# Kernel tuning notes

Measured on AMD Instinct MI355X. Metric: run time of the kernel, lower is better.

## Reference

```python
import jax, jax.numpy as jnp
import numpy as np
import math

# Model config (see init_kwargs)
E = 1024   # emb_size
H = 8      # ffwd_num_head
D = 128    # ffwd_head_size (E == H*D)
NE = 16    # ffwd_num_expert
A = 2      # ffwd_num_expert_active
S = 256    # ffwd_expert_size
B = 2      # batch_size_fwd
T = 2048   # context_window
NUM_BLOCK = 12


def setup_inputs() -> dict:
    key = jax.random.key(0)
    ks = jax.random.split(key, 5)
    x = jax.random.normal(ks[0], (B, T, E), jnp.float32)
    # fc_in_fused: Linear(E, 4E+NE, bias=False), torch weight shape (out,in)
    w_in = 0.02 * jax.random.normal(ks[1], (4 * E + NE, E), jnp.float32)
    # fc_out_fused: Linear(2E, E), std 0.02/sqrt(num_block)
    w_out = (0.02 / math.sqrt(NUM_BLOCK)) * jax.random.normal(ks[2], (E, 2 * E), jnp.float32)
    # k_ffwd/v_ffwd: original (1,H,NE*S,D); stored here as (NE,H,S,D) for per-expert scan
    k_ffwd = 0.02 * jax.random.normal(ks[3], (NE, H, S, D), jnp.float32)
    v_ffwd = 0.02 * jax.random.normal(ks[4], (NE, H, S, D), jnp.float32)
    return {"x": x, "w_in": w_in, "w_out": w_out, "k_ffwd": k_ffwd, "v_ffwd": v_ffwd}


def _rope(t):
    # Standard half-split RoPE, base 10000. t: (B,T,H,D)
    half = t.shape[-1] // 2
    inv_freq = 1.0 / (10000.0 ** (jnp.arange(half, dtype=jnp.float32) / half))
    ang = jnp.arange(t.shape[1], dtype=jnp.float32)[:, None] * inv_freq  # (T, half)
    cos = jnp.cos(ang)[None, :, None, :]
    sin = jnp.sin(ang)[None, :, None, :]
    t1, t2 = t[..., :half], t[..., half:]
    return jnp.concatenate([t1 * cos - t2 * sin, t1 * sin + t2 * cos], axis=-1)


def reference(x, w_in, w_out, k_ffwd, v_ffwd):
    Bx, Tx, _ = x.shape
    h = x @ w_in.T  # (B,T,4E+NE)
    q_f, q_a, k_a, v_a, router_logits = jnp.split(h, [E, 2 * E, 3 * E, 4 * E], axis=-1)

    # top-k routing (order of the k slots is irrelevant: outputs are summed)
    gate_logits, assign = jax.lax.top_k(router_logits, A)  # (B,T,A)
    gate = jax.nn.sigmoid(gate_logits)

    # --- attention half: causal softmax attention, scale 1/sqrt(D), with RoPE ---
    q = _rope(q_a.reshape(Bx, Tx, H, D))
    k = _rope(k_a.reshape(Bx, Tx, H, D))
    v = v_a.reshape(Bx, Tx, H, D)
    scores = jnp.einsum('bqhd,bkhd->bhqk', q, k) / math.sqrt(D)
    causal = jnp.tril(jnp.ones((Tx, Tx), dtype=bool))
    scores = jnp.where(causal, scores, -jnp.inf)
    p = jax.nn.softmax(scores, axis=-1)
    attn_out = jnp.einsum('bhqk,bkhd->bqhd', p, v).reshape(Bx, Tx, E)

    # --- MoE-FFN half, expressed as attention with score_mod log1p(gelu):
    # exp(lse)*softmax recovers sum_s (1+gelu(q.k_s)) v_s; subtracting sum_s v_s
    # leaves sum_s gelu(q.k_s) v_s over the assigned expert's slots. ---
    qf = q_f.reshape(Bx, Tx, H, D)

    def step(acc, ekv):
        e, ke, ve = ekv  # ke, ve: (H,S,D)
        s = jnp.einsum('bthd,hsd->bths', qf, ke)
        a = jax.nn.gelu(s, approximate=False)  # torch F.gelu default = exact erf
        o = jnp.einsum('bths,hsd->bthd', a, ve)
        g = jnp.sum(jnp.where(assign == e, gate, 0.0), axis=-1)  # (B,T)
        return acc + g[..., None, None] * o, None

    acc0 = jnp.zeros((Bx, Tx, H, D), x.dtype)
    ffwd_out, _ = jax.lax.scan(step, acc0, (jnp.arange(NE), k_ffwd, v_ffwd))
    ffwd_out = ffwd_out.reshape(Bx, Tx, E)

    out = jnp.concatenate([attn_out, ffwd_out], axis=-1) @ w_out.T  # (B,T,E)
    return out
```

## Files before the change

kernel.cpp:

```cpp
#include <hip/hip_runtime.h>
#include <hip/hip_bf16.h>
#include <math.h>

#define E 1024
#define NEXP 16
#define HH 8
#define DD 128
#define SS 256
#define BB 2
#define TT 2048
#define BT 4096

typedef __attribute__((ext_vector_type(8))) short bf16x8;
typedef __attribute__((ext_vector_type(4))) float f32x4;

#define GLDS16(g, s) __builtin_amdgcn_global_load_lds( \
    (const __attribute__((address_space(1))) void*)(g), \
    (__attribute__((address_space(3))) void*)(s), 16, 0, 0)

__device__ __forceinline__ ushort f2b(float f) {
    union { float f; unsigned u; } v; v.f = f;
    unsigned r = (v.u + 0x7FFFu + ((v.u >> 16) & 1u)) >> 16;
    return (ushort)r;
}
__device__ __forceinline__ float b2f(ushort u) {
    union { unsigned u; float f; } v; v.u = ((unsigned)u) << 16;
    return v.f;
}
__device__ __forceinline__ float gelu_fast(float x) {
    float u2 = x * x;
    float tu = x * (1.5957691216f + 0.0713548163f * u2);
    float e = __expf(tu);
    float sig = 1.f - __builtin_amdgcn_rcpf(e + 1.f);
    return x * sig;
}

__global__ void cvtk_swz(const float* __restrict__ in, ushort* __restrict__ outp,
                         int kshift, int n)
{
    int i = (blockIdx.x * blockDim.x + threadIdx.x) * 8;
    if (i >= n) return;
    int row = i >> kshift;
    int colb = (i - (row << kshift)) * 2;
    float4 f0 = *(const float4*)(in + i);
    float4 f1 = *(const float4*)(in + i + 4);
    ushort4 u0, u1;
    u0.x = f2b(f0.x); u0.y = f2b(f0.y); u0.z = f2b(f0.z); u0.w = f2b(f0.w);
    u1.x = f2b(f1.x); u1.y = f2b(f1.y); u1.z = f2b(f1.z); u1.w = f2b(f1.w);
    char* dst = (char*)outp + ((size_t)row << (kshift + 1)) + (colb ^ ((row & 7) << 4));
    *(ushort4*)dst = u0;
    *(ushort4*)(dst + 8) = u1;
}

template<int BF16OUT>
__global__ __launch_bounds__(256) void gemm_bf16(
    const ushort* __restrict__ A, int lda,
    const ushort* __restrict__ B, int ldb,
    void* __restrict__ Cv, int ldc, int K)
{
    __shared__ ushort As[128 * 64];
    __shared__ ushort Bs[128 * 64];
    const int t = threadIdx.x;
    const int l = t & 63, w = t >> 6;
    const int m0 = blockIdx.y * 128, n0 = blockIdx.x * 128;
    const int wr = w >> 1, wc = w & 1;
    const int fr = l & 15, fg = l >> 4;

    const int srow = w * 32 + (l >> 3);
    const int sboff = (l & 7) * 16;
    const char* Ag = (const char*)A + ((size_t)(m0 + srow) * lda) * 2 + sboff;
    const char* Bg = (const char*)B + ((size_t)(n0 + srow) * ldb) * 2 + sboff;
    const int aswz = (fr & 7) << 4;

    f32x4 acc[4][4];
    #pragma unroll
    for (int i = 0; i < 4; ++i)
        #pragma unroll
        for (int j = 0; j < 4; ++j) { acc[i][j][0]=0.f; acc[i][j][1]=0.f; acc[i][j][2]=0.f; acc[i][j][3]=0.f; }

    for (int k0b = 0; k0b < K * 2; k0b += 128) {
        #pragma unroll
        for (int i = 0; i < 4; ++i) {
            GLDS16(Ag + (size_t)(i * 8) * lda * 2 + k0b, (char*)As + (w * 32 + i * 8) * 128);
            GLDS16(Bg + (size_t)(i * 8) * ldb * 2 + k0b, (char*)Bs + (w * 32 + i * 8) * 128);
        }
        __syncthreads();
        #pragma unroll
        for (int ksub = 0; ksub < 2; ++ksub) {
            bf16x8 a[4], b[4];
            #pragma unroll
            for (int mi = 0; mi < 4; ++mi)
                a[mi] = *(const bf16x8*)((const char*)As + (wr * 64 + mi * 16 + fr) * 128 + ((ksub * 64 + fg * 16) ^ aswz));
            #pragma unroll
            for (int ni = 0; ni < 4; ++ni)
                b[ni] = *(const bf16x8*)((const char*)Bs + (wc * 64 + ni * 16 + fr) * 128 + ((ksub * 64 + fg * 16) ^ aswz));
            #pragma unroll
            for (int mi = 0; mi < 4; ++mi)
                #pragma unroll
                for (int ni = 0; ni < 4; ++ni)
                    acc[mi][ni] = __builtin_amdgcn_mfma_f32_16x16x32_bf16(a[mi], b[ni], acc[mi][ni], 0, 0, 0);
        }
        __syncthreads();
    }
    #pragma unroll
    for (int mi = 0; mi < 4; ++mi)
        #pragma unroll
        for (int ni = 0; ni < 4; ++ni) {
            const int row = m0 + wr * 64 + mi * 16 + fg * 4;
            const int col = n0 + wc * 64 + ni * 16 + fr;
            #pragma unroll
            for (int r = 0; r < 4; ++r) {
                if (BF16OUT)
                    ((ushort*)Cv)[(size_t)(row + r) * ldc + col] = f2b(acc[mi][ni][r]);
                else
                    ((float*)Cv)[(size_t)(row + r) * ldc + col] = acc[mi][ni][r];
            }
        }
}

__global__ __launch_bounds__(256) void gemm1_fused(
    const ushort* __restrict__ A, const ushort* __restrict__ B,
    ushort* __restrict__ hbq,
    ushort* __restrict__ qb, ushort* __restrict__ kb,
    ushort* __restrict__ vtb)
{
    __shared__ ushort sh[128 * 128];
    ushort* As = sh;
    ushort* Bs = sh + 128 * 64;
    const int t = threadIdx.x;
    const int l = t & 63, w = t >> 6;
    const int m0 = blockIdx.y * 128, n0 = blockIdx.x * 128;
    const int wr = w >> 1, wc = w & 1;
    const int fr = l & 15, fg = l >> 4;

    const int srow = w * 32 + (l >> 3);
    const int sboff = (l & 7) * 16;
    const char* Ag = (const char*)A + ((size_t)(m0 + srow) * 1024) * 2 + sboff;
    const char* Bg = (const char*)B + ((size_t)(n0 + srow) * 1024) * 2 + sboff;
    const int aswz = (fr & 7) << 4;

    f32x4 acc[4][4];
    #pragma unroll
    for (int i = 0; i < 4; ++i)
        #pragma unroll
        for (int j = 0; j < 4; ++j) { acc[i][j][0]=0.f; acc[i][j][1]=0.f; acc[i][j][2]=0.f; acc[i][j][3]=0.f; }

    for (int k0b = 0; k0b < 2048; k0b += 128) {
        #pragma unroll
        for (int i = 0; i < 4; ++i) {
            GLDS16(Ag + (size_t)(i * 8) * 2048 + k0b, (char*)As + (w * 32 + i * 8) * 128);
            GLDS16(Bg + (size_t)(i * 8) * 2048 + k0b, (char*)Bs + (w * 32 + i * 8) * 128);
        }
        __syncthreads();
        #pragma unroll
        for (int ksub = 0; ksub < 2; ++ksub) {
            bf16x8 a[4], b[4];
            #pragma unroll
            for (int mi = 0; mi < 4; ++mi)
                a[mi] = *(const bf16x8*)((const char*)As + (wr * 64 + mi * 16 + fr) * 128 + ((ksub * 64 + fg * 16) ^ aswz));
            #pragma unroll
            for (int ni = 0; ni < 4; ++ni)
                b[ni] = *(const bf16x8*)((const char*)Bs + (wc * 64 + ni * 16 + fr) * 128 + ((ksub * 64 + fg * 16) ^ aswz));
            #pragma unroll
            for (int mi = 0; mi < 4; ++mi)
                #pragma unroll
                for (int ni = 0; ni < 4; ++ni)
                    acc[mi][ni] = __builtin_amdgcn_mfma_f32_16x16x32_bf16(a[mi], b[ni], acc[mi][ni], 0, 0, 0);
        }
        __syncthreads();
    }

    const int region = blockIdx.x >> 3;
    const int hd = blockIdx.x & 7;

    if (region == 0) {
        #pragma unroll
        for (int mi = 0; mi < 4; ++mi)
            #pragma unroll
            for (int ni = 0; ni < 4; ++ni) {
                const int row = m0 + wr * 64 + mi * 16 + fg * 4;
                const int col = n0 + wc * 64 + ni * 16 + fr;
                #pragma unroll
                for (int r = 0; r < 4; ++r)
                    hbq[(size_t)(row + r) * 1024 + col] = f2b(acc[mi][ni][r]);
            }
    } else if (region == 3) {
        #pragma unroll
        for (int mi = 0; mi < 4; ++mi) {
            const int rowg = m0 + wr * 64 + mi * 16 + fg * 4;
            const int tok = rowg & 2047, bt = rowg >> 11;
            const int bh = bt * 8 + hd;
            #pragma unroll
            for (int ni = 0; ni < 4; ++ni) {
                const int d = wc * 64 + ni * 16 + fr;
                ushort4 u;
                u.x = f2b(acc[mi][ni][0]); u.y = f2b(acc[mi][ni][1]);
                u.z = f2b(acc[mi][ni][2]); u.w = f2b(acc[mi][ni][3]);
                char* dst = (char*)vtb + (size_t)(bh * 128 + d) * 4096
                          + (tok >> 6) * 128 + ((2 * (tok & 63)) ^ ((d & 7) << 4));
                *(ushort4*)dst = u;
            }
        }
    } else {
        #pragma unroll
        for (int mi = 0; mi < 4; ++mi)
            #pragma unroll
            for (int ni = 0; ni < 4; ++ni) {
                const int rl = wr * 64 + mi * 16 + fg * 4;
                const int cl = wc * 64 + ni * 16 + fr;
                #pragma unroll
                for (int r = 0; r < 4; ++r)
                    sh[(rl + r) * 128 + cl] = f2b(acc[mi][ni][r]);
            }
        __syncthreads();
        ushort* outb = (region == 1) ? qb : kb;
        #pragma unroll
        for (int it = 0; it < 4; ++it) {
            const int item = it * 256 + t;
            const int rloc = item >> 3, g = item & 7;
            const int rowg = m0 + rloc;
            const int tok = rowg & 2047, bt = rowg >> 11;
            const int sw = (tok & 7) << 4;
            char* rowbase = (char*)outb + ((size_t)((bt * 8 + hd) * 2048 + tok)) * 256;
            ushort lo[8], hi[8];
            #pragma unroll
            for (int jj = 0; jj < 8; ++jj) {
                const int j = g * 8 + jj;
                float t1 = b2f(sh[rloc * 128 + j]);
                float t2 = b2f(sh[rloc * 128 + 64 + j]);
                float invf = __expf(-(float)j * (9.210340371976184f / 64.f));
                float ang = (float)tok * invf;
                float s, c;
                sincosf(ang, &s, &c);
                lo[jj] = f2b(t1 * c - t2 * s);
                hi[jj] = f2b(t1 * s + t2 * c);
            }
            *(ushort4*)(rowbase + ((16 * g) ^ sw))        = *(ushort4*)&lo[0];
            *(ushort4*)(rowbase + (((16 * g) ^ sw) + 8))  = *(ushort4*)&lo[4];
            *(ushort4*)(rowbase + ((16 * g + 128) ^ sw))       = *(ushort4*)&hi[0];
            *(ushort4*)(rowbase + (((16 * g + 128) ^ sw) + 8)) = *(ushort4*)&hi[4];
        }
    }
}

__global__ __launch_bounds__(256) void router_logits(
    const float* __restrict__ x, const float* __restrict__ w_in,
    float* __restrict__ gval, int* __restrict__ eidx, ushort* __restrict__ xb)
{
    const int m = blockIdx.x * 4 + (threadIdx.x >> 6);
    const int lane = threadIdx.x & 63;

    const float* xp = x + (size_t)m * 1024 + lane * 4;
    float4 xv0 = *(const float4*)(xp);
    float4 xv1 = *(const float4*)(xp + 256);
    float4 xv2 = *(const float4*)(xp + 512);
    float4 xv3 = *(const float4*)(xp + 768);

    {
        const int swrow = (m & 7) << 4;
        char* xrow = (char*)xb + (size_t)m * 2048;
        ushort4 u;
        u.x = f2b(xv0.x); u.y = f2b(xv0.y); u.z = f2b(xv0.z); u.w = f2b(xv0.w);
        *(ushort4*)(xrow + ((lane * 8 + 0 * 512) ^ swrow)) = u;
        u.x = f2b(xv1.x); u.y = f2b(xv1.y); u.z = f2b(xv1.z); u.w = f2b(xv1.w);
        *(ushort4*)(xrow + ((lane * 8 + 1 * 512) ^ swrow)) = u;
        u.x = f2b(xv2.x); u.y = f2b(xv2.y); u.z = f2b(xv2.z); u.w = f2b(xv2.w);
        *(ushort4*)(xrow + ((lane * 8 + 2 * 512) ^ swrow)) = u;
        u.x = f2b(xv3.x); u.y = f2b(xv3.y); u.z = f2b(xv3.z); u.w = f2b(xv3.w);
        *(ushort4*)(xrow + ((lane * 8 + 3 * 512) ^ swrow)) = u;
    }

    float p[16];
    #pragma unroll
    for (int e = 0; e < 16; ++e) {
        const float* wp = w_in + (size_t)(4096 + e) * 1024 + lane * 4;
        float4 w0 = *(const float4*)(wp);
        float4 w1 = *(const float4*)(wp + 256);
        float4 w2 = *(const float4*)(wp + 512);
        float4 w3 = *(const float4*)(wp + 768);
        float s0 = xv0.x * w0.x + xv0.y * w0.y + xv0.z * w0.z + xv0.w * w0.w;
        float s1 = xv1.x * w1.x + xv1.y * w1.y + xv1.z * w1.z + xv1.w * w1.w;
        float s2 = xv2.x * w2.x + xv2.y * w2.y + xv2.z * w2.z + xv2.w * w2.w;
        float s3 = xv3.x * w3.x + xv3.y * w3.y + xv3.z * w3.z + xv3.w * w3.w;
        p[e] = (s0 + s1) + (s2 + s3);
    }
    #pragma unroll
    for (int d = 1; d < 64; d <<= 1) {
        #pragma unroll
        for (int e = 0; e < 16; ++e)
            p[e] += __shfl_xor(p[e], d);
    }
    float best = -1e30f; int bi = 0;
    #pragma unroll
    for (int e = 0; e < 16; ++e)
        if (p[e] > best) { best = p[e]; bi = e; }
    float best2 = -1e30f; int bi2 = 0;
    #pragma unroll
    for (int e = 0; e < 16; ++e)
        if (e != bi && p[e] > best2) { best2 = p[e]; bi2 = e; }

    if (lane == 0) {
        gval[m * 2 + 0] = 1.f / (1.f + __expf(-best));
        gval[m * 2 + 1] = 1.f / (1.f + __expf(-best2));
        eidx[m * 2 + 0] = bi;
        eidx[m * 2 + 1] = bi2;
    }
}

__global__ __launch_bounds__(256) void build_lists(
    const int* __restrict__ eidx,
    int* __restrict__ counts, int* __restrict__ plist)
{
    const int e = blockIdx.x;
    const int t = threadIdx.x;
    const int w = t >> 6, lane = t & 63;
    __shared__ int wbase[4];
    __shared__ int running;
    if (t == 0) running = 0;
    __syncthreads();
    for (int c = 0; c < 2 * BT; c += 256) {
        const int p = c + t;
        const bool match = (eidx[p] == e);
        unsigned long long mask = __ballot(match);
        int lpre = __popcll(mask & ((lane == 63) ? 0x7FFFFFFFFFFFFFFFull
                                                 : ((1ull << lane) - 1ull)));
        if (lane == 0) wbase[w] = __popcll(mask);
        __syncthreads();
        int pre = running;
        #pragma unroll
        for (int i = 0; i < 4; ++i) if (i < w) pre += wbase[i];
        const int tot = wbase[0] + wbase[1] + wbase[2] + wbase[3];
        if (match) plist[e * BT + pre + lpre] = p;
        __syncthreads();
        if (t == 0) running += tot;
        __syncthreads();
    }
    if (t == 0) counts[e] = running;
}

__global__ __launch_bounds__(256) void cvt_kv(
    const float* __restrict__ kf, const float* __restrict__ vf,
    ushort* __restrict__ kfb, ushort* __restrict__ vtf)
{
    __shared__ float T[64][132];
    int eh = blockIdx.y, st = blockIdx.x;
    int s0 = st * 64;
    int t = threadIdx.x;
    const float* kbp = kf + (size_t)eh * SS * DD + (size_t)s0 * DD;
    const float* vbp = vf + (size_t)eh * SS * DD + (size_t)s0 * DD;
    for (int i = t; i < 64 * 32; i += 256) {
        int r = i >> 5, c4 = i & 31;
        float4 f = *(const float4*)(kbp + (size_t)r * DD + c4 * 4);
        ushort4 u;
        u.x = f2b(f.x); u.y = f2b(f.y); u.z = f2b(f.z); u.w = f2b(f.w);
        *(ushort4*)((char*)kfb + ((size_t)eh * 256 + s0 + r) * 256 + ((c4 * 8) ^ ((r & 7) << 4))) = u;
    }
    for (int i = t; i < 64 * 32; i += 256) {
        int r = i >> 5, c4 = i & 31;
        float4 f = *(const float4*)(vbp + (size_t)r * DD + c4 * 4);
        T[r][c4 * 4 + 0] = f.x; T[r][c4 * 4 + 1] = f.y;
        T[r][c4 * 4 + 2] = f.z; T[r][c4 * 4 + 3] = f.w;
    }
    __syncthreads();
    int g = t >> 4, fr = t & 15;
    #pragma unroll
    for (int dd = 0; dd < 8; ++dd) {
        int d = g + dd * 16;
        ushort4 u;
        u.x = f2b(T[4 * fr + 0][d]); u.y = f2b(T[4 * fr + 1][d]);
        u.z = f2b(T[4 * fr + 2][d]); u.w = f2b(T[4 * fr + 3][d]);
        size_t ob = ((size_t)eh * 128 + d) * 512 + s0 * 2;
        *(ushort4*)((char*)vtf + ob + ((8 * fr) ^ ((d & 7) << 4))) = u;
    }
}

__global__ __launch_bounds__(512, 1) void attn_mfma(
    const ushort* __restrict__ qb, const ushort* __restrict__ kb,
    const ushort* __restrict__ vtb, ushort* __restrict__ catb)
{
    __shared__ ushort Ks[2][128 * 128];
    __shared__ ushort Vs[2][128 * 128];
    __shared__ ushort Ps[8][16 * 72];
    __shared__ float  LlS[8][16];

    const int t = threadIdx.x, l = t & 63, w = t >> 6;
    const int fr = l & 15, fg = l >> 4;
    const int wl = w & 3, hh = w >> 2;
    const int lin = blockIdx.x;
    const int bh = (lin & 7) * 2 + (lin >> 7);
    const int tpair = (lin >> 3) & 15;
    const int swz = (fr & 7) << 4;
    ushort* Pw = (ushort*)Ps[w];

    #pragma unroll 1
    for (int pass = 0; pass < 2; ++pass) {
        const int qt = pass ? (31 - tpair) : tpair;
        const int qbase = qt * 64;
        const int nkt = (qt + 2) >> 1;
        const int qg = qbase + wl * 16 + fg * 4;

        bf16x8 qreg[4];
        {
            const char* qrow = (const char*)qb + ((size_t)(bh * 2048 + qbase + wl * 16 + fr)) * 256;
            #pragma unroll
            for (int ks = 0; ks < 4; ++ks)
                qreg[ks] = *(const bf16x8*)(qrow + ((ks * 64 + fg * 16) ^ swz));
        }
        {
            const char* ksrc = (const char*)kb + ((size_t)(bh * 2048 + w * 16)) * 256;
            const char* vsrc = (const char*)vtb + ((size_t)(bh * 128 + w * 16)) * 4096;
            #pragma unroll
            for (int i = 0; i < 4; ++i) {
                GLDS16(ksrc + (size_t)(i * 4 + (l >> 4)) * 256 + (l & 15) * 16,
                       (char*)Ks[0] + (w * 16 + i * 4) * 256);
                GLDS16(vsrc + (size_t)(i * 4 + (l >> 4)) * 4096 + (l & 15) * 16,
                       (char*)Vs[0] + (w * 16 + i * 4) * 256);
            }
        }

        f32x4 po[8];
        #pragma unroll
        for (int i = 0; i < 8; ++i) { po[i][0]=0.f; po[i][1]=0.f; po[i][2]=0.f; po[i][3]=0.f; }
        float lrow[4] = {0.f, 0.f, 0.f, 0.f};

        asm volatile("s_waitcnt vmcnt(0)" ::: "memory");
        __syncthreads();

        for (int kt = 0; kt < nkt; ++kt) {
            const int cur = kt & 1;
            if (kt + 1 < nkt) {
                const int kvn = (kt + 1) * 128;
                const char* ksrc = (const char*)kb + ((size_t)(bh * 2048 + kvn + w * 16)) * 256;
                const char* vsrc = (const char*)vtb + ((size_t)(bh * 128 + w * 16)) * 4096 + kvn * 2;
                #pragma unroll
                for (int i = 0; i < 4; ++i) {
                    GLDS16(ksrc + (size_t)(i * 4 + (l >> 4)) * 256 + (l & 15) * 16,
                           (char*)Ks[cur ^ 1] + (w * 16 + i * 4) * 256);
                    GLDS16(vsrc + (size_t)(i * 4 + (l >> 4)) * 4096 + (l & 15) * 16,
                           (char*)Vs[cur ^ 1] + (w * 16 + i * 4) * 256);
                }
            }
            const int kvb = kt * 128;

            f32x4 s[4];
            #pragma unroll
            for (int i = 0; i < 4; ++i) { s[i][0]=0.f; s[i][1]=0.f; s[i][2]=0.f; s[i][3]=0.f; }
            __builtin_amdgcn_s_setprio(1);
            #pragma unroll
            for (int ks = 0; ks < 4; ++ks) {
                #pragma unroll
                for (int fn = 0; fn < 4; ++fn) {
                    const int brow = hh * 64 + fn * 16 + fr;
                    bf16x8 bb = *(const bf16x8*)((const char*)Ks[cur] + brow * 256 + ((ks * 64 + fg * 16) ^ swz));
                    s[fn] = __builtin_amdgcn_mfma_f32_16x16x32_bf16(qreg[ks], bb, s[fn], 0, 0, 0);
                }
            }
            __builtin_amdgcn_s_setprio(0);

            const int colbase = kvb + hh * 64;
            const bool needmask = (colbase + 64 > qbase + wl * 16);
            float ps[4] = {0.f, 0.f, 0.f, 0.f};
            #pragma unroll
            for (int fn = 0; fn < 4; ++fn)
                #pragma unroll
                for (int r = 0; r < 4; ++r) {
                    float v = s[fn][r] * 0.08838834764831845f;
                    bool masked = needmask && (colbase + fn * 16 + fr > qg + r);
                    float p = masked ? 0.f : __expf(v);
                    ps[r] += p;
                    Pw[(fg * 4 + r) * 72 + fn * 16 + fr] = f2b(p);
                }
            #pragma unroll
            for (int r = 0; r < 4; ++r) {
                float s2 = ps[r];
                s2 += __shfl_xor(s2, 1);
                s2 += __shfl_xor(s2, 2);
                s2 += __shfl_xor(s2, 4);
                s2 += __shfl_xor(s2, 8);
                lrow[r] += s2;
            }

            asm volatile("s_waitcnt lgkmcnt(0)" ::: "memory");
            __builtin_amdgcn_sched_barrier(0);

            __builtin_amdgcn_s_setprio(1);
            #pragma unroll
            for (int ks2 = 0; ks2 < 2; ++ks2) {
                bf16x8 pa = *(const bf16x8*)((const char*)Pw + fr * 144 + ks2 * 64 + fg * 16);
                #pragma unroll
                for (int fn2 = 0; fn2 < 8; ++fn2) {
                    const int vrow = fn2 * 16 + fr;
                    bf16x8 bv = *(const bf16x8*)((const char*)Vs[cur] + vrow * 256 + ((hh * 128 + ks2 * 64 + fg * 16) ^ swz));
                    po[fn2] = __builtin_amdgcn_mfma_f32_16x16x32_bf16(pa, bv, po[fn2], 0, 0, 0);
                }
            }
            __builtin_amdgcn_s_setprio(0);

            asm volatile("s_waitcnt vmcnt(0)" ::: "memory");
            __syncthreads();
        }

        if (fr == 0) {
            #pragma unroll
            for (int r = 0; r < 4; ++r)
                LlS[w][fg * 4 + r] = lrow[r];
        }
        __syncthreads();
        float linv[4];
        #pragma unroll
        for (int r = 0; r < 4; ++r)
            linv[r] = 1.f / (lrow[r] + LlS[w ^ 4][fg * 4 + r]);
        float* PO = (float*)&Ks[0][0];
        if (hh == 1) {
            #pragma unroll
            for (int fn2 = 0; fn2 < 8; ++fn2)
                #pragma unroll
                for (int r = 0; r < 4; ++r)
                    PO[(wl * 16 + fg * 4 + r) * 128 + fn2 * 16 + fr] = po[fn2][r];
        }
        __syncthreads();
        if (hh == 0) {
            const int mg = (bh >> 3) * 2048 + qbase + wl * 16 + fg * 4;
            #pragma unroll
            for (int r = 0; r < 4; ++r) {
                const int rswz = ((mg + r) & 7) << 4;
                #pragma unroll
                for (int fn2 = 0; fn2 < 8; ++fn2) {
                    float v = po[fn2][r] + PO[(wl * 16 + fg * 4 + r) * 128 + fn2 * 16 + fr];
                    int colb = ((bh & 7) * 128 + fn2 * 16 + fr) * 2;
                    *(ushort*)((char*)catb + (size_t)(mg + r) * 4096 + (colb ^ rswz)) = f2b(v * linv[r]);
                }
            }
        }
        __syncthreads();
    }
}

__global__ __launch_bounds__(256, 1) void ffn_mfma2(
    const ushort* __restrict__ hbq,
    const float* __restrict__ gv,
    const int* __restrict__ counts,
    const int* __restrict__ plist,
    const ushort* __restrict__ kfb, const ushort* __restrict__ vtf,
    ushort* __restrict__ pairout)
{
    __shared__ ushort Ks[256 * 128];
    __shared__ ushort Vs[128 * 256];
    __shared__ ushort Qs[64 * 128];
    __shared__ ushort Ps[4][16 * 72];

    const int t = threadIdx.x, l = t & 63, w = t >> 6;
    const int fr = l & 15, fg = l >> 4;
    const int half = blockIdx.x, hd = blockIdx.y, e = blockIdx.z;
    const int eh = e * HH + hd;
    const int n_e = counts[e];

    {
        const char* kbase = (const char*)kfb + (size_t)eh * 65536;
        const char* vbase = (const char*)vtf + (size_t)eh * 65536;
        #pragma unroll
        for (int i = 0; i < 16; ++i) {
            GLDS16(kbase + (w * 64 + i * 4) * 256 + l * 16, (char*)Ks + (w * 64 + i * 4) * 256);
            GLDS16(vbase + w * 16384 + i * 1024 + l * 16, (char*)Vs + w * 16384 + i * 1024);
        }
    }
    __syncthreads();

    const int arow = w * 16 + fr;
    const int aswz = (arow & 7) << 4;
    ushort* Pw = (ushort*)Ps[w];
    const int rl4 = l >> 4;
    const int lb = (l & 15) * 16;

    for (int tb = half * 64; tb < n_e; tb += 128) {
        #pragma unroll
        for (int i = 0; i < 4; ++i) {
            int row = w * 16 + i * 4 + rl4;
            int gr = tb + row;
            int p = plist[e * BT + min(gr, n_e - 1)];
            int m = p >> 1;
            const char* src = (const char*)hbq + (size_t)m * 2048 + hd * 256 + (lb ^ ((row & 7) << 4));
            GLDS16(src, (char*)Qs + (w * 16 + i * 4) * 256);
        }
        asm volatile("s_waitcnt vmcnt(0)" ::: "memory");

        f32x4 po[8];
        #pragma unroll
        for (int i = 0; i < 8; ++i) { po[i][0]=0.f; po[i][1]=0.f; po[i][2]=0.f; po[i][3]=0.f; }

        #pragma unroll
        for (int kt = 0; kt < 4; ++kt) {
            const int kvb = kt * 64;
            f32x4 sA[4];
            #pragma unroll
            for (int i = 0; i < 4; ++i) { sA[i][0]=0.f; sA[i][1]=0.f; sA[i][2]=0.f; sA[i][3]=0.f; }
            #pragma unroll
            for (int ks = 0; ks < 4; ++ks) {
                bf16x8 aa = *(const bf16x8*)((const char*)Qs + arow * 256 + ((ks * 64 + fg * 16) ^ aswz));
                #pragma unroll
                for (int fn = 0; fn < 4; ++fn) {
                    const int brow = kvb + fn * 16 + fr;
                    bf16x8 bb = *(const bf16x8*)((const char*)Ks + brow * 256 + ((ks * 64 + fg * 16) ^ ((brow & 7) << 4)));
                    sA[fn] = __builtin_amdgcn_mfma_f32_16x16x32_bf16(aa, bb, sA[fn], 0, 0, 0);
                }
            }
            #pragma unroll
            for (int fn = 0; fn < 4; ++fn)
                #pragma unroll
                for (int r = 0; r < 4; ++r)
                    Pw[(fg * 4 + r) * 72 + fn * 16 + fr] = f2b(gelu_fast(sA[fn][r]));
            asm volatile("s_waitcnt lgkmcnt(0)" ::: "memory");
            #pragma unroll
            for (int ks2 = 0; ks2 < 2; ++ks2) {
                bf16x8 pa = *(const bf16x8*)((const char*)Pw + fr * 144 + ks2 * 64 + fg * 16);
                #pragma unroll
                for (int fn2 = 0; fn2 < 8; ++fn2) {
                    const int vrow = fn2 * 16 + fr;
                    bf16x8 bv = *(const bf16x8*)((const char*)Vs + vrow * 512 + kt * 128 + ((ks2 * 64 + fg * 16) ^ ((vrow & 7) << 4)));
                    po[fn2] = __builtin_amdgcn_mfma_f32_16x16x32_bf16(pa, bv, po[fn2], 0, 0, 0);
                }
            }
        }
        const int rloc = w * 16 + fg * 4;
        #pragma unroll
        for (int r = 0; r < 4; ++r) {
            int gr = tb + rloc + r;
            if (gr < n_e) {
                int p = plist[e * BT + gr];
                float g = gv[p];
                #pragma unroll
                for (int fn2 = 0; fn2 < 8; ++fn2)
                    pairout[(size_t)p * 1024 + hd * DD + fn2 * 16 + fr] = f2b(g * po[fn2][r]);
            }
        }
    }
}

__global__ void combine_kernel(const ushort* __restrict__ po, ushort* __restrict__ catb)
{
    int i = blockIdx.x * blockDim.x + threadIdx.x;
    if (i >= BT * 128) return;
    int m = i >> 7, c = i & 127;
    const ushort* a = po + (size_t)(2 * m) * 1024 + c * 8;
    const ushort* b = po + (size_t)(2 * m + 1) * 1024 + c * 8;
    ushort4 a0 = *(const ushort4*)a, a1 = *(const ushort4*)(a + 4);
    ushort4 b0 = *(const ushort4*)b, b1 = *(const ushort4*)(b + 4);
    ushort4 o0, o1;
    o0.x = f2b(b2f(a0.x) + b2f(b0.x)); o0.y = f2b(b2f(a0.y) + b2f(b0.y));
    o0.z = f2b(b2f(a0.z) + b2f(b0.z)); o0.w = f2b(b2f(a0.w) + b2f(b0.w));
    o1.x = f2b(b2f(a1.x) + b2f(b1.x)); o1.y = f2b(b2f(a1.y) + b2f(b1.y));
    o1.z = f2b(b2f(a1.z) + b2f(b1.z)); o1.w = f2b(b2f(a1.w) + b2f(b1.w));
    char* dst = (char*)catb + (size_t)m * 4096 + 2048 + ((c * 16) ^ ((m & 7) << 4));
    *(ushort4*)dst = o0;
    *(ushort4*)(dst + 8) = o1;
}

extern "C" void kernel_launch(void* const* d_in, const int* in_sizes, int n_in,
                              void* d_out, int out_size, void* d_ws, size_t ws_size,
                              hipStream_t stream)
{
    const float* x     = (const float*)d_in[0];
    const float* w_in  = (const float*)d_in[1];
    const float* w_out = (const float*)d_in[2];
    const float* kf    = (const float*)d_in[3];
    const float* vf    = (const float*)d_in[4];
    float* out = (float*)d_out;

    char* W = (char*)d_ws;
    ushort* hbq     = (ushort*)(W + 0);
    ushort* xb      = (ushort*)(W + 33554432);
    ushort* wib     = (ushort*)(W + 41943040);
    ushort* kfb     = xb;
    ushort* vtf     = wib;
    ushort* wob     = (ushort*)(W + 50331648);
    ushort* qb2     = (ushort*)(W + 54525952);
    ushort* kb2     = (ushort*)(W + 62914560);
    ushort* vtb     = (ushort*)(W + 71303168);
    ushort* catb    = (ushort*)(W + 79691776);
    ushort* pairout = (ushort*)(W + 96468992);
    float*  gv      = (float*)(W + 113246208);
    int*    counts  = (int*)(W + 113278976);
    int*    plist   = (int*)(W + 113279040);
    int*    eidx    = (int*)(W + 113541184);

    cvtk_swz<<<2048, 256, 0, stream>>>(w_in, wib, 10, 4096 * 1024);
    cvtk_swz<<<1024, 256, 0, stream>>>(w_out, wob, 11, 1024 * 2048);

    router_logits<<<BT / 4, 256, 0, stream>>>(x, w_in, gv, eidx, xb);
    build_lists<<<NEXP, 256, 0, stream>>>(eidx, counts, plist);

    gemm1_fused<<<dim3(32, 32), 256, 0, stream>>>(xb, wib, hbq, qb2, kb2, vtb);

    cvt_kv<<<dim3(4, NEXP * HH), 256, 0, stream>>>(kf, vf, kfb, vtf);

    attn_mfma<<<dim3(256), 512, 0, stream>>>(qb2, kb2, vtb, catb);

    ffn_mfma2<<<dim3(2, HH, NEXP), 256, 0, stream>>>(hbq, gv, counts, plist, kfb, vtf, pairout);
    combine_kernel<<<2048, 256, 0, stream>>>(pairout, catb);

    gemm_bf16<0><<<dim3(8, 32), 256, 0, stream>>>(catb, 2048, wob, 2048, out, 1024, 2048);
}
```

Baseline: 234.1 us.

## Widen gemm1 tile to 128x256 and apply RoPE directly from registers

The fused input GEMM now uses a 128x256 output tile, so each wave covers a full 128-wide head and A-tile loads are reused across twice as many columns, halving the grid. Because each wave holds both halves of a head, the RoPE epilogue rotates straight from accumulator registers and drops the LDS staging round-trip and its extra barrier. In exchange it doubles the accumulator registers, which may reduce occupancy, and writes q/k with scattered 2-byte stores instead of vectorized 8-byte stores. Only 512 blocks remain, which may underfill the GPU.

Result: slower. 809.0 us (+245.6%).

```diff
diff --git a/kernel.cpp b/kernel.cpp
--- a/kernel.cpp
+++ b/kernel.cpp
@@ -124,62 +124,63 @@
     ushort* __restrict__ qb, ushort* __restrict__ kb,
     ushort* __restrict__ vtb)
 {
-    __shared__ ushort sh[128 * 128];
-    ushort* As = sh;
-    ushort* Bs = sh + 128 * 64;
+    __shared__ ushort As[128 * 64];
+    __shared__ ushort Bs[256 * 64];
     const int t = threadIdx.x;
     const int l = t & 63, w = t >> 6;
-    const int m0 = blockIdx.y * 128, n0 = blockIdx.x * 128;
+    const int m0 = blockIdx.y * 128, n0 = blockIdx.x * 256;
     const int wr = w >> 1, wc = w & 1;
     const int fr = l & 15, fg = l >> 4;
 
-    const int srow = w * 32 + (l >> 3);
+    const int lrow = l >> 3;
     const int sboff = (l & 7) * 16;
-    const char* Ag = (const char*)A + ((size_t)(m0 + srow) * 1024) * 2 + sboff;
-    const char* Bg = (const char*)B + ((size_t)(n0 + srow) * 1024) * 2 + sboff;
+    const char* Ag = (const char*)A + ((size_t)(m0 + w * 32 + lrow) * 1024) * 2 + sboff;
+    const char* Bg = (const char*)B + ((size_t)(n0 + w * 64 + lrow) * 1024) * 2 + sboff;
     const int aswz = (fr & 7) << 4;
 
-    f32x4 acc[4][4];
+    f32x4 acc[4][8];
     #pragma unroll
     for (int i = 0; i < 4; ++i)
         #pragma unroll
-        for (int j = 0; j < 4; ++j) { acc[i][j][0]=0.f; acc[i][j][1]=0.f; acc[i][j][2]=0.f; acc[i][j][3]=0.f; }
+        for (int j = 0; j < 8; ++j) { acc[i][j][0]=0.f; acc[i][j][1]=0.f; acc[i][j][2]=0.f; acc[i][j][3]=0.f; }
 
     for (int k0b = 0; k0b < 2048; k0b += 128) {
         #pragma unroll
-        for (int i = 0; i < 4; ++i) {
+        for (int i = 0; i < 4; ++i)
             GLDS16(Ag + (size_t)(i * 8) * 2048 + k0b, (char*)As + (w * 32 + i * 8) * 128);
-            GLDS16(Bg + (size_t)(i * 8) * 2048 + k0b, (char*)Bs + (w * 32 + i * 8) * 128);
-        }
+        #pragma unroll
+        for (int i = 0; i < 8; ++i)
+            GLDS16(Bg + (size_t)(i * 8) * 2048 + k0b, (char*)Bs + (w * 64 + i * 8) * 128);
         __syncthreads();
         #pragma unroll
         for (int ksub = 0; ksub < 2; ++ksub) {
-            bf16x8 a[4], b[4];
+            bf16x8 a[4], b[8];
             #pragma unroll
             for (int mi = 0; mi < 4; ++mi)
                 a[mi] = *(const bf16x8*)((const char*)As + (wr * 64 + mi * 16 + fr) * 128 + ((ksub * 64 + fg * 16) ^ aswz));
             #pragma unroll
-            for (int ni = 0; ni < 4; ++ni)
-                b[ni] = *(const bf16x8*)((const char*)Bs + (wc * 64 + ni * 16 + fr) * 128 + ((ksub * 64 + fg * 16) ^ aswz));
+            for (int ni = 0; ni < 8; ++ni)
+                b[ni] = *(const bf16x8*)((const char*)Bs + (wc * 128 + ni * 16 + fr) * 128 + ((ksub * 64 + fg * 16) ^ aswz));
             #pragma unroll
             for (int mi = 0; mi < 4; ++mi)
                 #pragma unroll
-                for (int ni = 0; ni < 4; ++ni)
+                for (int ni = 0; ni < 8; ++ni)
                     acc[mi][ni] = __builtin_amdgcn_mfma_f32_16x16x32_bf16(a[mi], b[ni], acc[mi][ni], 0, 0, 0);
         }
         __syncthreads();
     }
 
-    const int region = blockIdx.x >> 3;
-    const int hd = blockIdx.x & 7;
+    const int region = blockIdx.x >> 2;
+    const int creg = blockIdx.x & 3;
+    const int hd = creg * 2 + wc;
 
     if (region == 0) {
         #pragma unroll
         for (int mi = 0; mi < 4; ++mi)
             #pragma unroll
-            for (int ni = 0; ni < 4; ++ni) {
+            for (int ni = 0; ni < 8; ++ni) {
                 const int row = m0 + wr * 64 + mi * 16 + fg * 4;
-                const int col = n0 + wc * 64 + ni * 16 + fr;
+                const int col = n0 + wc * 128 + ni * 16 + fr;
                 #pragma unroll
                 for (int r = 0; r < 4; ++r)
                     hbq[(size_t)(row + r) * 1024 + col] = f2b(acc[mi][ni][r]);
@@ -191,8 +192,8 @@
             const int tok = rowg & 2047, bt = rowg >> 11;
             const int bh = bt * 8 + hd;
             #pragma unroll
-            for (int ni = 0; ni < 4; ++ni) {
-                const int d = wc * 64 + ni * 16 + fr;
+            for (int ni = 0; ni < 8; ++ni) {
+                const int d = ni * 16 + fr;
                 ushort4 u;
                 u.x = f2b(acc[mi][ni][0]); u.y = f2b(acc[mi][ni][1]);
                 u.z = f2b(acc[mi][ni][2]); u.w = f2b(acc[mi][ni][3]);
@@ -202,43 +203,32 @@
             }
         }
     } else {
-        #pragma unroll
-        for (int mi = 0; mi < 4; ++mi)
-            #pragma unroll
-            for (int ni = 0; ni < 4; ++ni) {
-                const int rl = wr * 64 + mi * 16 + fg * 4;
-                const int cl = wc * 64 + ni * 16 + fr;
-                #pragma unroll
-                for (int r = 0; r < 4; ++r)
-                    sh[(rl + r) * 128 + cl] = f2b(acc[mi][ni][r]);
-            }
-        __syncthreads();
         ushort* outb = (region == 1) ? qb : kb;
-        #pragma unroll
-        for (int it = 0; it < 4; ++it) {
-            const int item = it * 256 + t;
-            const int rloc = item >> 3, g = item & 7;
-            const int rowg = m0 + rloc;
-            const int tok = rowg & 2047, bt = rowg >> 11;
-            const int sw = (tok & 7) << 4;
-            char* rowbase = (char*)outb + ((size_t)((bt * 8 + hd) * 2048 + tok)) * 256;
-            ushort lo[8], hi[8];
-            #pragma unroll
-            for (int jj = 0; jj < 8; ++jj) {
-                const int j = g * 8 + jj;
-                float t1 = b2f(sh[rloc * 128 + j]);
-                float t2 = b2f(sh[rloc * 128 + 64 + j]);
-                float invf = __expf(-(float)j * (9.210340371976184f / 64.f));
-                float ang = (float)tok * invf;
-                float s, c;
-                sincosf(ang, &s, &c);
-                lo[jj] = f2b(t1 * c - t2 * s);
-                hi[jj] = f2b(t1 * s + t2 * c);
-            }
-            *(ushort4*)(rowbase + ((16 * g) ^ sw))        = *(ushort4*)&lo[0];
-            *(ushort4*)(rowbase + (((16 * g) ^ sw) + 8))  = *(ushort4*)&lo[4];
-            *(ushort4*)(rowbase + ((16 * g + 128) ^ sw))       = *(ushort4*)&hi[0];
-            *(ushort4*)(rowbase + (((16 * g + 128) ^ sw) + 8)) = *(ushort4*)&hi[4];
+        float invfs[4];
+        #pragma unroll
+        for (int ni = 0; ni < 4; ++ni)
+            invfs[ni] = __expf(-(float)(ni * 16 + fr) * (9.210340371976184f / 64.f));
+        #pragma unroll
+        for (int mi = 0; mi < 4; ++mi) {
+            const int rowg0 = m0 + wr * 64 + mi * 16 + fg * 4;
+            #pragma unroll
+            for (int r = 0; r < 4; ++r) {
+                const int rowg = rowg0 + r;
+                const int tok = rowg & 2047, bt = rowg >> 11;
+                const int sw = (tok & 7) << 4;
+                char* rowbase = (char*)outb + ((size_t)((bt * 8 + hd) * 2048 + tok)) * 256;
+                #pragma unroll
+                for (int ni = 0; ni < 4; ++ni) {
+                    const int j = ni * 16 + fr;
+                    float t1 = acc[mi][ni][r];
+                    float t2 = acc[mi][ni + 4][r];
+                    float ang = (float)tok * invfs[ni];
+                    float s, c;
+                    sincosf(ang, &s, &c);
+                    *(ushort*)(rowbase + ((2 * j) ^ sw))         = f2b(t1 * c - t2 * s);
+                    *(ushort*)(rowbase + ((2 * j + 128) ^ sw))   = f2b(t1 * s + t2 * c);
+                }
+            }
         }
     }
 }
@@ -689,7 +679,7 @@
     router_logits<<<BT / 4, 256, 0, stream>>>(x, w_in, gv, eidx, xb);
     build_lists<<<NEXP, 256, 0, stream>>>(eidx, counts, plist);
 
-    gemm1_fused<<<dim3(32, 32), 256, 0, stream>>>(xb, wib, hbq, qb2, kb2, vtb);
+    gemm1_fused<<<dim3(16, 32), 256, 0, stream>>>(xb, wib, hbq, qb2, kb2, vtb);
 
     cvt_kv<<<dim3(4, NEXP * HH), 256, 0, stream>>>(kf, vf, kfb, vtf);
 
```

## Merge weight/KV conversion kernels and fuse expert-pair combine into output GEMM

Applied to the files above, without the earlier changes.

Three conversion launches (w_in, w_out, k/v) are merged into one prep kernel; kfb/vtf get dedicated workspace so k/v conversion no longer waits on gemm1. The combine kernel is removed, and the final GEMM now sums the two expert-pair rows of pairout while loading the second half of its K dimension into shared memory. This removes two launches and a round trip through catb's FFN half. The cost is that the FFN half of the GEMM uses synchronous register loads instead of async global-to-LDS loads, which may stall the MFMA loop.

New measurement: 238.0 us. Within noise of the previous version (+1.7%).

```diff
diff --git a/kernel.cpp b/kernel.cpp
--- a/kernel.cpp
+++ b/kernel.cpp
@@ -35,87 +35,64 @@
     return x * sig;
 }
 
-__global__ void cvtk_swz(const float* __restrict__ in, ushort* __restrict__ outp,
-                         int kshift, int n)
+__global__ __launch_bounds__(256) void prep(
+    const float* __restrict__ w_in, const float* __restrict__ w_out,
+    const float* __restrict__ kf, const float* __restrict__ vf,
+    ushort* __restrict__ wib, ushort* __restrict__ wob,
+    ushort* __restrict__ kfb, ushort* __restrict__ vtf)
 {
-    int i = (blockIdx.x * blockDim.x + threadIdx.x) * 8;
-    if (i >= n) return;
-    int row = i >> kshift;
-    int colb = (i - (row << kshift)) * 2;
-    float4 f0 = *(const float4*)(in + i);
-    float4 f1 = *(const float4*)(in + i + 4);
-    ushort4 u0, u1;
-    u0.x = f2b(f0.x); u0.y = f2b(f0.y); u0.z = f2b(f0.z); u0.w = f2b(f0.w);
-    u1.x = f2b(f1.x); u1.y = f2b(f1.y); u1.z = f2b(f1.z); u1.w = f2b(f1.w);
-    char* dst = (char*)outp + ((size_t)row << (kshift + 1)) + (colb ^ ((row & 7) << 4));
-    *(ushort4*)dst = u0;
-    *(ushort4*)(dst + 8) = u1;
-}
-
-template<int BF16OUT>
-__global__ __launch_bounds__(256) void gemm_bf16(
-    const ushort* __restrict__ A, int lda,
-    const ushort* __restrict__ B, int ldb,
-    void* __restrict__ Cv, int ldc, int K)
-{
-    __shared__ ushort As[128 * 64];
-    __shared__ ushort Bs[128 * 64];
+    __shared__ float T[64][132];
+    const int bx = blockIdx.x;
     const int t = threadIdx.x;
-    const int l = t & 63, w = t >> 6;
-    const int m0 = blockIdx.y * 128, n0 = blockIdx.x * 128;
-    const int wr = w >> 1, wc = w & 1;
-    const int fr = l & 15, fg = l >> 4;
-
-    const int srow = w * 32 + (l >> 3);
-    const int sboff = (l & 7) * 16;
-    const char* Ag = (const char*)A + ((size_t)(m0 + srow) * lda) * 2 + sboff;
-    const char* Bg = (const char*)B + ((size_t)(n0 + srow) * ldb) * 2 + sboff;
-    const int aswz = (fr & 7) << 4;
-
-    f32x4 acc[4][4];
+
+    if (bx < 3072) {
+        const float* in;
+        ushort* outp;
+        int kshift, i;
+        if (bx < 2048) { in = w_in;  outp = wib; kshift = 10; i = (bx * 256 + t) * 8; }
+        else           { in = w_out; outp = wob; kshift = 11; i = ((bx - 2048) * 256 + t) * 8; }
+        int row = i >> kshift;
+        int colb = (i - (row << kshift)) * 2;
+        float4 f0 = *(const float4*)(in + i);
+        float4 f1 = *(const float4*)(in + i + 4);
+        ushort4 u0, u1;
+        u0.x = f2b(f0.x); u0.y = f2b(f0.y); u0.z = f2b(f0.z); u0.w = f2b(f0.w);
+        u1.x = f2b(f1.x); u1.y = f2b(f1.y); u1.z = f2b(f1.z); u1.w = f2b(f1.w);
+        char* dst = (char*)outp + ((size_t)row << (kshift + 1)) + (colb ^ ((row & 7) << 4));
+        *(ushort4*)dst = u0;
+        *(ushort4*)(dst + 8) = u1;
+        return;
+    }
+
+    const int idx = bx - 3072;
+    const int st = idx & 3, eh = idx >> 2;
+    const int s0 = st * 64;
+    const float* kbp = kf + (size_t)eh * SS * DD + (size_t)s0 * DD;
+    const float* vbp = vf + (size_t)eh * SS * DD + (size_t)s0 * DD;
+    for (int i = t; i < 64 * 32; i += 256) {
+        int r = i >> 5, c4 = i & 31;
+        float4 f = *(const float4*)(kbp + (size_t)r * DD + c4 * 4);
+        ushort4 u;
+        u.x = f2b(f.x); u.y = f2b(f.y); u.z = f2b(f.z); u.w = f2b(f.w);
+        *(ushort4*)((char*)kfb + ((size_t)eh * 256 + s0 + r) * 256 + ((c4 * 8) ^ ((r & 7) << 4))) = u;
+    }
+    for (int i = t; i < 64 * 32; i += 256) {
+        int r = i >> 5, c4 = i & 31;
+        float4 f = *(const float4*)(vbp + (size_t)r * DD + c4 * 4);
+        T[r][c4 * 4 + 0] = f.x; T[r][c4 * 4 + 1] = f.y;
+        T[r][c4 * 4 + 2] = f.z; T[r][c4 * 4 + 3] = f.w;
+    }
+    __syncthreads();
+    int g = t >> 4, fr = t & 15;
     #pragma unroll
-    for (int i = 0; i < 4; ++i)
-        #pragma unroll
-        for (int j = 0; j < 4; ++j) { acc[i][j][0]=0.f; acc[i][j][1]=0.f; acc[i][j][2]=0.f; acc[i][j][3]=0.f; }
-
-    for (int k0b = 0; k0b < K * 2; k0b += 128) {
-        #pragma unroll
-        for (int i = 0; i < 4; ++i) {
-            GLDS16(Ag + (size_t)(i * 8) * lda * 2 + k0b, (char*)As + (w * 32 + i * 8) * 128);
-            GLDS16(Bg + (size_t)(i * 8) * ldb * 2 + k0b, (char*)Bs + (w * 32 + i * 8) * 128);
-        }
-        __syncthreads();
-        #pragma unroll
-        for (int ksub = 0; ksub < 2; ++ksub) {
-            bf16x8 a[4], b[4];
-            #pragma unroll
-            for (int mi = 0; mi < 4; ++mi)
-                a[mi] = *(const bf16x8*)((const char*)As + (wr * 64 + mi * 16 + fr) * 128 + ((ksub * 64 + fg * 16) ^ aswz));
-            #pragma unroll
-            for (int ni = 0; ni < 4; ++ni)
-                b[ni] = *(const bf16x8*)((const char*)Bs + (wc * 64 + ni * 16 + fr) * 128 + ((ksub * 64 + fg * 16) ^ aswz));
-            #pragma unroll
-            for (int mi = 0; mi < 4; ++mi)
-                #pragma unroll
-                for (int ni = 0; ni < 4; ++ni)
-                    acc[mi][ni] = __builtin_amdgcn_mfma_f32_16x16x32_bf16(a[mi], b[ni], acc[mi][ni], 0, 0, 0);
-        }
-        __syncthreads();
-    }
-    #pragma unroll
-    for (int mi = 0; mi < 4; ++mi)
-        #pragma unroll
-        for (int ni = 0; ni < 4; ++ni) {
-            const int row = m0 + wr * 64 + mi * 16 + fg * 4;
-            const int col = n0 + wc * 64 + ni * 16 + fr;
-            #pragma unroll
-            for (int r = 0; r < 4; ++r) {
-                if (BF16OUT)
-                    ((ushort*)Cv)[(size_t)(row + r) * ldc + col] = f2b(acc[mi][ni][r]);
-                else
-                    ((float*)Cv)[(size_t)(row + r) * ldc + col] = acc[mi][ni][r];
-            }
-        }
+    for (int dd = 0; dd < 8; ++dd) {
+        int d = g + dd * 16;
+        ushort4 u;
+        u.x = f2b(T[4 * fr + 0][d]); u.y = f2b(T[4 * fr + 1][d]);
+        u.z = f2b(T[4 * fr + 2][d]); u.w = f2b(T[4 * fr + 3][d]);
+        size_t ob = ((size_t)eh * 128 + d) * 512 + s0 * 2;
+        *(ushort4*)((char*)vtf + ob + ((8 * fr) ^ ((d & 7) << 4))) = u;
+    }
 }
 
 __global__ __launch_bounds__(256) void gemm1_fused(
@@ -338,42 +315,6 @@
     if (t == 0) counts[e] = running;
 }
 
-__global__ __launch_bounds__(256) void cvt_kv(
-    const float* __restrict__ kf, const float* __restrict__ vf,
-    ushort* __restrict__ kfb, ushort* __restrict__ vtf)
-{
-    __shared__ float T[64][132];
-    int eh = blockIdx.y, st = blockIdx.x;
-    int s0 = st * 64;
-    int t = threadIdx.x;
-    const float* kbp = kf + (size_t)eh * SS * DD + (size_t)s0 * DD;
-    const float* vbp = vf + (size_t)eh * SS * DD + (size_t)s0 * DD;
-    for (int i = t; i < 64 * 32; i += 256) {
-        int r = i >> 5, c4 = i & 31;
-        float4 f = *(const float4*)(kbp + (size_t)r * DD + c4 * 4);
-        ushort4 u;
-        u.x = f2b(f.x); u.y = f2b(f.y); u.z = f2b(f.z); u.w = f2b(f.w);
-        *(ushort4*)((char*)kfb + ((size_t)eh * 256 + s0 + r) * 256 + ((c4 * 8) ^ ((r & 7) << 4))) = u;
-    }
-    for (int i = t; i < 64 * 32; i += 256) {
-        int r = i >> 5, c4 = i & 31;
-        float4 f = *(const float4*)(vbp + (size_t)r * DD + c4 * 4);
-        T[r][c4 * 4 + 0] = f.x; T[r][c4 * 4 + 1] = f.y;
-        T[r][c4 * 4 + 2] = f.z; T[r][c4 * 4 + 3] = f.w;
-    }
-    __syncthreads();
-    int g = t >> 4, fr = t & 15;
-    #pragma unroll
-    for (int dd = 0; dd < 8; ++dd) {
-        int d = g + dd * 16;
-        ushort4 u;
-        u.x = f2b(T[4 * fr + 0][d]); u.y = f2b(T[4 * fr + 1][d]);
-        u.z = f2b(T[4 * fr + 2][d]); u.w = f2b(T[4 * fr + 3][d]);
-        size_t ob = ((size_t)eh * 128 + d) * 512 + s0 * 2;
-        *(ushort4*)((char*)vtf + ob + ((8 * fr) ^ ((d & 7) << 4))) = u;
-    }
-}
-
 __global__ __launch_bounds__(512, 1) void attn_mfma(
     const ushort* __restrict__ qb, const ushort* __restrict__ kb,
     const ushort* __restrict__ vtb, ushort* __restrict__ catb)
@@ -636,23 +577,89 @@
     }
 }
 
-__global__ void combine_kernel(const ushort* __restrict__ po, ushort* __restrict__ catb)
+__global__ __launch_bounds__(256) void gemm2_fused(
+    const ushort* __restrict__ A,
+    const ushort* __restrict__ B,
+    const ushort* __restrict__ pairout,
+    float* __restrict__ C)
 {
-    int i = blockIdx.x * blockDim.x + threadIdx.x;
-    if (i >= BT * 128) return;
-    int m = i >> 7, c = i & 127;
-    const ushort* a = po + (size_t)(2 * m) * 1024 + c * 8;
-    const ushort* b = po + (size_t)(2 * m + 1) * 1024 + c * 8;
-    ushort4 a0 = *(const ushort4*)a, a1 = *(const ushort4*)(a + 4);
-    ushort4 b0 = *(const ushort4*)b, b1 = *(const ushort4*)(b + 4);
-    ushort4 o0, o1;
-    o0.x = f2b(b2f(a0.x) + b2f(b0.x)); o0.y = f2b(b2f(a0.y) + b2f(b0.y));
-    o0.z = f2b(b2f(a0.z) + b2f(b0.z)); o0.w = f2b(b2f(a0.w) + b2f(b0.w));
-    o1.x = f2b(b2f(a1.x) + b2f(b1.x)); o1.y = f2b(b2f(a1.y) + b2f(b1.y));
-    o1.z = f2b(b2f(a1.z) + b2f(b1.z)); o1.w = f2b(b2f(a1.w) + b2f(b1.w));
-    char* dst = (char*)catb + (size_t)m * 4096 + 2048 + ((c * 16) ^ ((m & 7) << 4));
-    *(ushort4*)dst = o0;
-    *(ushort4*)(dst + 8) = o1;
+    __shared__ ushort As[128 * 64];
+    __shared__ ushort Bs[128 * 64];
+    const int t = threadIdx.x;
+    const int l = t & 63, w = t >> 6;
+    const int m0 = blockIdx.y * 128, n0 = blockIdx.x * 128;
+    const int wr = w >> 1, wc = w & 1;
+    const int fr = l & 15, fg = l >> 4;
+
+    const int srow = w * 32 + (l >> 3);
+    const int sboff = (l & 7) * 16;
+    const char* Ag = (const char*)A + ((size_t)(m0 + srow) * 2048) * 2 + sboff;
+    const char* Bg = (const char*)B + ((size_t)(n0 + srow) * 2048) * 2 + sboff;
+    const int aswz = (fr & 7) << 4;
+
+    f32x4 acc[4][4];
+    #pragma unroll
+    for (int i = 0; i < 4; ++i)
+        #pragma unroll
+        for (int j = 0; j < 4; ++j) { acc[i][j][0]=0.f; acc[i][j][1]=0.f; acc[i][j][2]=0.f; acc[i][j][3]=0.f; }
+
+    for (int k0b = 0; k0b < 4096; k0b += 128) {
+        if (k0b < 2048) {
+            #pragma unroll
+            for (int i = 0; i < 4; ++i)
+                GLDS16(Ag + (size_t)(i * 8) * 4096 + k0b, (char*)As + (w * 32 + i * 8) * 128);
+        } else {
+            const int kk = k0b - 2048;
+            #pragma unroll
+            for (int i = 0; i < 4; ++i) {
+                const int r = w * 32 + i * 8 + (l >> 3);
+                const int rg = m0 + r;
+                const char* pa = (const char*)pairout + (size_t)(2 * rg) * 2048 + kk + (l & 7) * 16;
+                ushort4 a0 = *(const ushort4*)pa;
+                ushort4 a1 = *(const ushort4*)(pa + 8);
+                ushort4 b0 = *(const ushort4*)(pa + 2048);
+                ushort4 b1 = *(const ushort4*)(pa + 2056);
+                ushort4 o0, o1;
+                o0.x = f2b(b2f(a0.x) + b2f(b0.x)); o0.y = f2b(b2f(a0.y) + b2f(b0.y));
+                o0.z = f2b(b2f(a0.z) + b2f(b0.z)); o0.w = f2b(b2f(a0.w) + b2f(b0.w));
+                o1.x = f2b(b2f(a1.x) + b2f(b1.x)); o1.y = f2b(b2f(a1.y) + b2f(b1.y));
+                o1.z = f2b(b2f(a1.z) + b2f(b1.z)); o1.w = f2b(b2f(a1.w) + b2f(b1.w));
+                char* dst = (char*)As + r * 128 + (sboff ^ ((r & 7) << 4));
+                *(ushort4*)dst = o0;
+                *(ushort4*)(dst + 8) = o1;
+            }
+        }
+        #pragma unroll
+        for (int i = 0; i < 4; ++i)
+            GLDS16(Bg + (size_t)(i * 8) * 4096 + k0b, (char*)Bs + (w * 32 + i * 8) * 128);
+        __syncthreads();
+        #pragma unroll
+        for (int ksub = 0; ksub < 2; ++ksub) {
+            bf16x8 a[4], b[4];
+            #pragma unroll
+            for (int mi = 0; mi < 4; ++mi)
+                a[mi] = *(const bf16x8*)((const char*)As + (wr * 64 + mi * 16 + fr) * 128 + ((ksub * 64 + fg * 16) ^ aswz));
+            #pragma unroll
+            for (int ni = 0; ni < 4; ++ni)
+                b[ni] = *(const bf16x8*)((const char*)Bs + (wc * 64 + ni * 16 + fr) * 128 + ((ksub * 64 + fg * 16) ^ aswz));
+            #pragma unroll
+            for (int mi = 0; mi < 4; ++mi)
+                #pragma unroll
+                for (int ni = 0; ni < 4; ++ni)
+                    acc[mi][ni] = __builtin_amdgcn_mfma_f32_16x16x32_bf16(a[mi], b[ni], acc[mi][ni], 0, 0, 0);
+        }
+        __syncthreads();
+    }
+    #pragma unroll
+    for (int mi = 0; mi < 4; ++mi)
+        #pragma unroll
+        for (int ni = 0; ni < 4; ++ni) {
+            const int row = m0 + wr * 64 + mi * 16 + fg * 4;
+            const int col = n0 + wc * 64 + ni * 16 + fr;
+            #pragma unroll
+            for (int r = 0; r < 4; ++r)
+                C[(size_t)(row + r) * 1024 + col] = acc[mi][ni][r];
+        }
 }
 
 extern "C" void kernel_launch(void* const* d_in, const int* in_sizes, int n_in,
@@ -670,8 +677,6 @@
     ushort* hbq     = (ushort*)(W + 0);
     ushort* xb      = (ushort*)(W + 33554432);
     ushort* wib     = (ushort*)(W + 41943040);
-    ushort* kfb     = xb;
-    ushort* vtf     = wib;
     ushort* wob     = (ushort*)(W + 50331648);
     ushort* qb2     = (ushort*)(W + 54525952);
     ushort* kb2     = (ushort*)(W + 62914560);
@@ -682,21 +687,19 @@
     int*    counts  = (int*)(W + 113278976);
     int*    plist   = (int*)(W + 113279040);
     int*    eidx    = (int*)(W + 113541184);
-
-    cvtk_swz<<<2048, 256, 0, stream>>>(w_in, wib, 10, 4096 * 1024);
-    cvtk_swz<<<1024, 256, 0, stream>>>(w_out, wob, 11, 1024 * 2048);
+    ushort* kfb     = (ushort*)(W + 113573952);
+    ushort* vtf     = (ushort*)(W + 121962560);
+
+    prep<<<3584, 256, 0, stream>>>(w_in, w_out, kf, vf, wib, wob, kfb, vtf);
 
     router_logits<<<BT / 4, 256, 0, stream>>>(x, w_in, gv, eidx, xb);
     build_lists<<<NEXP, 256, 0, stream>>>(eidx, counts, plist);
 
     gemm1_fused<<<dim3(32, 32), 256, 0, stream>>>(xb, wib, hbq, qb2, kb2, vtb);
 
-    cvt_kv<<<dim3(4, NEXP * HH), 256, 0, stream>>>(kf, vf, kfb, vtf);
-
     attn_mfma<<<dim3(256), 512, 0, stream>>>(qb2, kb2, vtb, catb);
 
     ffn_mfma2<<<dim3(2, HH, NEXP), 256, 0, stream>>>(hbq, gv, counts, plist, kfb, vtf, pairout);
-    combine_kernel<<<2048, 256, 0, stream>>>(pairout, catb);
-
-    gemm_bf16<0><<<dim3(8, 32), 256, 0, stream>>>(catb, 2048, wob, 2048, out, 1024, 2048);
-}
+
+    gemm2_fused<<<dim3(8, 32), 256, 0, stream>>>(catb, wob, pairout, out);
+}
```
